# Kernel optimization log

Hardware: AMD Instinct MI355X
Metric: run time of the kernel (lower is better)

## Reference

```python
import jax, jax.numpy as jnp
import numpy as np

B, H, S, D = 2, 16, 2048, 64

def setup_inputs() -> dict:
    key = jax.random.key(0)
    kq, kk, kv, km = jax.random.split(key, 4)
    Q = jax.random.normal(kq, (B, H, S, D), dtype=jnp.float32)
    K = jax.random.normal(kk, (B, H, S, D), dtype=jnp.float32)
    V = jax.random.normal(kv, (B, H, S, D), dtype=jnp.float32)
    # padding-style boolean mask, broadcast over heads; True = masked out
    attn_mask = jax.random.randint(km, (B, 1, S, S), 0, 2).astype(jnp.bool_)
    return {"Q": Q, "K": K, "V": V, "attn_mask": attn_mask}

def reference(Q, K, V, attn_mask):
    d = Q.shape[-1]
    scale = 1.0 / np.sqrt(d).astype(np.float32)
    # [B,H,S,S] scores
    scores = jnp.einsum('bhqd,bhkd->bhqk', Q, K) * scale
    scores = jnp.where(attn_mask, jnp.float32(-1e9), scores)
    attn = jax.nn.softmax(scores, axis=-1)
    context = jnp.einsum('bhqk,bhkd->bhqd', attn, V)
    return context
```

## Files before the change

### kernel.cpp

```cpp
#include <hip/hip_runtime.h>

#define B_ 2
#define H_ 16
#define S_ 2048
#define D_ 64
#define BK 32
#define NKT (S_ / BK)
#define QSCALE 0.18033688011112042f

#define KSD 36
#define VTD 18
#define KS_SZ (BK * KSD)
#define VT_SZ (D_ * VTD)

typedef __attribute__((ext_vector_type(4))) float  float4v;
typedef __attribute__((ext_vector_type(2))) _Float16 half2v;
typedef __attribute__((ext_vector_type(4))) _Float16 half4v;
typedef __attribute__((ext_vector_type(8))) _Float16 half8v;
typedef __attribute__((ext_vector_type(2))) __fp16 fp16x2;
typedef __attribute__((ext_vector_type(2))) unsigned uint2v;

union H2U { half2v h; fp16x2 g; unsigned u; };
union H4U { half4v h4; half2v h2[2]; fp16x2 g2[2]; uint2v u2; };
union H8U { half8v h8; half2v h2[4]; fp16x2 g2[4]; };

__device__ __forceinline__ unsigned pkh(float a, float b) {
    H2U c; c.g = __builtin_amdgcn_cvt_pkrtz(a, b);
    return c.u;
}
__device__ __forceinline__ float fexp2(float x) {
#if __has_builtin(__builtin_amdgcn_exp2f)
    return __builtin_amdgcn_exp2f(x);
#else
    return exp2f(x);
#endif
}

struct Stage { float4 k0, k1, va, vb; };

__device__ __forceinline__ void stage_load(const float* __restrict__ Kg,
                                           const float* __restrict__ Vg,
                                           int kk, int dd, int kp, Stage& s) {
    s.k0 = *(const float4*)(Kg + (size_t)kk * D_ + dd);
    s.k1 = *(const float4*)(Kg + (size_t)(kk + 16) * D_ + dd);
    s.va = *(const float4*)(Vg + (size_t)(2 * kp) * D_ + dd);
    s.vb = *(const float4*)(Vg + (size_t)(2 * kp + 1) * D_ + dd);
}

__device__ __forceinline__ void stage_store(unsigned* KsB, unsigned* VtB,
                                            int kwa, int kwb, const int* vw,
                                            const Stage& s) {
    *(uint2v*)&KsB[kwa] = (uint2v){ pkh(s.k0.x, s.k0.y), pkh(s.k0.z, s.k0.w) };
    *(uint2v*)&KsB[kwb] = (uint2v){ pkh(s.k1.x, s.k1.y), pkh(s.k1.z, s.k1.w) };
    VtB[vw[0]] = pkh(s.va.x, s.vb.x);
    VtB[vw[1]] = pkh(s.va.y, s.vb.y);
    VtB[vw[2]] = pkh(s.va.z, s.vb.z);
    VtB[vw[3]] = pkh(s.va.w, s.vb.w);
}

__global__ __launch_bounds__(256, 4)
void attn_flash_st(const float* __restrict__ Q, const float* __restrict__ K,
                   const float* __restrict__ V, const int* __restrict__ mask,
                   float* __restrict__ out)
{
    __shared__ unsigned KsAll[2 * KS_SZ];
    __shared__ unsigned VtAll[2 * VT_SZ];

    const int tid  = threadIdx.x;
    const int lane = tid & 63;
    const int wave = tid >> 6;
    const int l15  = lane & 15;
    const int quad = lane >> 4;
    const int bh   = blockIdx.y;
    const int b    = bh / H_;
    const int qbase = blockIdx.x * 64 + wave * 16;
    const size_t qkv = (size_t)bh * S_ * D_;

    half8v qf[2];
    {
        const float* qrow = Q + qkv + (size_t)(qbase + l15) * D_ + quad * 8;
        #pragma unroll
        for (int dc = 0; dc < 2; ++dc) {
            float4 f0 = *(const float4*)(qrow + dc * 32);
            float4 f1 = *(const float4*)(qrow + dc * 32 + 4);
            H8U u;
            u.g2[0] = __builtin_amdgcn_cvt_pkrtz(f0.x * QSCALE, f0.y * QSCALE);
            u.g2[1] = __builtin_amdgcn_cvt_pkrtz(f0.z * QSCALE, f0.w * QSCALE);
            u.g2[2] = __builtin_amdgcn_cvt_pkrtz(f1.x * QSCALE, f1.y * QSCALE);
            u.g2[3] = __builtin_amdgcn_cvt_pkrtz(f1.z * QSCALE, f1.w * QSCALE);
            qf[dc] = u.h8;
        }
    }

    const int kk = tid >> 4;
    const int dd = (tid & 15) * 4;
    const int kwa = kk * KSD + (tid & 15) * 2;
    const int kwb = (kk + 16) * KSD + (tid & 15) * 2;
    int vw[4];
    #pragma unroll
    for (int m = 0; m < 4; ++m)
        vw[m] = (dd + m) * VTD + (kk ^ (((dd + m) & 7) << 1));

    int kroff[2][2];
    #pragma unroll
    for (int t = 0; t < 2; ++t)
        #pragma unroll
        for (int dc = 0; dc < 2; ++dc)
            kroff[t][dc] = (t * 16 + l15) * KSD + dc * 16 + quad * 4;
    const int vswz = (l15 & 7) << 1;
    const int p0x[2] = { (quad * 2) ^ vswz, (8 + quad * 2) ^ vswz };
    int vrow[4];
    #pragma unroll
    for (int nb = 0; nb < 4; ++nb) vrow[nb] = (nb * 16 + l15) * VTD;

    const int* mrow = mask + (size_t)b * S_ * S_ + (size_t)(qbase + l15) * S_ + quad * 4;

    float m_run = -INFINITY, l_run = 0.0f;
    float4v o[4];
    #pragma unroll
    for (int nb = 0; nb < 4; ++nb) o[nb] = (float4v){0.f, 0.f, 0.f, 0.f};

    const float* Kg0 = K + qkv;
    const float* Vg0 = V + qkv;

    Stage cur;
    stage_load(Kg0, Vg0, kk, dd, kk, cur);
    stage_store(KsAll, VtAll, kwa, kwb, vw, cur);
    __syncthreads();

    for (int kt = 0; kt < NKT; ++kt) {
        const int buf = kt & 1;
        const unsigned* KsB = KsAll + buf * KS_SZ;
        const unsigned* VtB = VtAll + buf * VT_SZ;

        const int ktn = (kt + 1 < NKT) ? kt + 1 : NKT - 1;
        Stage nxt;
        stage_load(Kg0 + (size_t)ktn * BK * D_, Vg0 + (size_t)ktn * BK * D_, kk, dd, kk, nxt);

        float4v st0 = (float4v){0.f,0.f,0.f,0.f}, st1 = st0;
        {
            half8v kf;
            kf = *(const half8v*)&KsB[kroff[0][0]];
            st0 = __builtin_amdgcn_mfma_f32_16x16x32_f16(kf, qf[0], st0, 0, 0, 0);
            kf = *(const half8v*)&KsB[kroff[0][1]];
            st0 = __builtin_amdgcn_mfma_f32_16x16x32_f16(kf, qf[1], st0, 0, 0, 0);
            kf = *(const half8v*)&KsB[kroff[1][0]];
            st1 = __builtin_amdgcn_mfma_f32_16x16x32_f16(kf, qf[0], st1, 0, 0, 0);
            kf = *(const half8v*)&KsB[kroff[1][1]];
            st1 = __builtin_amdgcn_mfma_f32_16x16x32_f16(kf, qf[1], st1, 0, 0, 0);
        }

        const int4 mk0 = *(const int4*)(mrow);
        const int4 mk1 = *(const int4*)(mrow + 16);
        mrow += BK;
        st0.x = mk0.x ? -1e9f : st0.x;  st0.y = mk0.y ? -1e9f : st0.y;
        st0.z = mk0.z ? -1e9f : st0.z;  st0.w = mk0.w ? -1e9f : st0.w;
        st1.x = mk1.x ? -1e9f : st1.x;  st1.y = mk1.y ? -1e9f : st1.y;
        st1.z = mk1.z ? -1e9f : st1.z;  st1.w = mk1.w ? -1e9f : st1.w;

        float mx = fmaxf(fmaxf(fmaxf(st0.x, st0.y), fmaxf(st0.z, st0.w)),
                         fmaxf(fmaxf(st1.x, st1.y), fmaxf(st1.z, st1.w)));
        mx = fmaxf(mx, __shfl_xor(mx, 16, 64));
        mx = fmaxf(mx, __shfl_xor(mx, 32, 64));
        const float mnew = fmaxf(m_run, mx);
        const float alpha = fexp2(m_run - mnew);
        m_run = mnew;

        st0.x = fexp2(st0.x - mnew); st0.y = fexp2(st0.y - mnew);
        st0.z = fexp2(st0.z - mnew); st0.w = fexp2(st0.w - mnew);
        st1.x = fexp2(st1.x - mnew); st1.y = fexp2(st1.y - mnew);
        st1.z = fexp2(st1.z - mnew); st1.w = fexp2(st1.w - mnew);

        float ls = ((st0.x + st0.y) + (st0.z + st0.w)) +
                   ((st1.x + st1.y) + (st1.z + st1.w));
        ls += __shfl_xor(ls, 16, 64);
        ls += __shfl_xor(ls, 32, 64);
        l_run = l_run * alpha + ls;

        #pragma unroll
        for (int nb = 0; nb < 4; ++nb) o[nb] *= alpha;

        H4U pf0u, pf1u;
        pf0u.g2[0] = __builtin_amdgcn_cvt_pkrtz(st0.x, st0.y);
        pf0u.g2[1] = __builtin_amdgcn_cvt_pkrtz(st0.z, st0.w);
        pf1u.g2[0] = __builtin_amdgcn_cvt_pkrtz(st1.x, st1.y);
        pf1u.g2[1] = __builtin_amdgcn_cvt_pkrtz(st1.z, st1.w);

        #pragma unroll
        for (int nb = 0; nb < 4; ++nb) {
            H4U vf;
            vf.u2 = *(const uint2v*)&VtB[vrow[nb] + p0x[0]];
            o[nb] = __builtin_amdgcn_mfma_f32_16x16x16f16(vf.h4, pf0u.h4, o[nb], 0, 0, 0);
            vf.u2 = *(const uint2v*)&VtB[vrow[nb] + p0x[1]];
            o[nb] = __builtin_amdgcn_mfma_f32_16x16x16f16(vf.h4, pf1u.h4, o[nb], 0, 0, 0);
        }

        stage_store((unsigned*)KsAll + (buf ^ 1) * KS_SZ,
                    (unsigned*)VtAll + (buf ^ 1) * VT_SZ, kwa, kwb, vw, nxt);
        __syncthreads();
    }

    const float inv = 1.0f / l_run;
    float* orow = out + qkv + (size_t)(qbase + l15) * D_ + quad * 4;
    #pragma unroll
    for (int nb = 0; nb < 4; ++nb) {
        float4 ov = { o[nb].x * inv, o[nb].y * inv, o[nb].z * inv, o[nb].w * inv };
        *(float4*)(orow + nb * 16) = ov;
    }
}

extern "C" void kernel_launch(void* const* d_in, const int* in_sizes, int n_in,
                              void* d_out, int out_size, void* d_ws, size_t ws_size,
                              hipStream_t stream) {
    const float* Q    = (const float*)d_in[0];
    const float* K    = (const float*)d_in[1];
    const float* V    = (const float*)d_in[2];
    const int*   mask = (const int*)d_in[3];
    float* out = (float*)d_out;

    dim3 grid(S_ / 64, B_ * H_);
    dim3 block(256);
    attn_flash_st<<<grid, block, 0, stream>>>(Q, K, V, mask, out);
}
```

Before: 233.7 us.

## Deepen K/V global prefetch to two tiles and prefetch mask one tile ahead

Global loads of K/V are issued two tiles ahead into alternating register stages, and mask loads are issued one iteration early so their latency overlaps the MFMA work. The V-transpose LDS swizzle is changed to depend on the column block rather than the low row bits, and the per-block read offsets are precomputed. __syncthreads is replaced by an inline s_waitcnt lgkmcnt(0) plus s_barrier that skips waiting on outstanding global loads. This raises register pressure from the extra staged tile and depends on the new swizzle staying consistent between writes and reads.

```diff
diff --git a/kernel.cpp b/kernel.cpp
--- a/kernel.cpp
+++ b/kernel.cpp
@@ -22,7 +22,7 @@
 
 union H2U { half2v h; fp16x2 g; unsigned u; };
 union H4U { half4v h4; half2v h2[2]; fp16x2 g2[2]; uint2v u2; };
-union H8U { half8v h8; half2v h2[4]; fp16x2 g2[4]; };
+union H8U { half8v h8; fp16x2 g2[4]; };
 
 __device__ __forceinline__ unsigned pkh(float a, float b) {
     H2U c; c.g = __builtin_amdgcn_cvt_pkrtz(a, b);
@@ -36,15 +36,19 @@
 #endif
 }
 
+__device__ __forceinline__ void wg_barrier() {
+    asm volatile("s_waitcnt lgkmcnt(0)\n\ts_barrier" ::: "memory");
+}
+
 struct Stage { float4 k0, k1, va, vb; };
 
 __device__ __forceinline__ void stage_load(const float* __restrict__ Kg,
                                            const float* __restrict__ Vg,
-                                           int kk, int dd, int kp, Stage& s) {
+                                           int kk, int dd, Stage& s) {
     s.k0 = *(const float4*)(Kg + (size_t)kk * D_ + dd);
     s.k1 = *(const float4*)(Kg + (size_t)(kk + 16) * D_ + dd);
-    s.va = *(const float4*)(Vg + (size_t)(2 * kp) * D_ + dd);
-    s.vb = *(const float4*)(Vg + (size_t)(2 * kp + 1) * D_ + dd);
+    s.va = *(const float4*)(Vg + (size_t)(2 * kk) * D_ + dd);
+    s.vb = *(const float4*)(Vg + (size_t)(2 * kk + 1) * D_ + dd);
 }
 
 __device__ __forceinline__ void stage_store(unsigned* KsB, unsigned* VtB,
@@ -68,9 +72,9 @@
 
     const int tid  = threadIdx.x;
     const int lane = tid & 63;
-    const int wave = tid >> 6;
     const int l15  = lane & 15;
     const int quad = lane >> 4;
+    const int wave = tid >> 6;
     const int bh   = blockIdx.y;
     const int b    = bh / H_;
     const int qbase = blockIdx.x * 64 + wave * 16;
@@ -99,7 +103,7 @@
     int vw[4];
     #pragma unroll
     for (int m = 0; m < 4; ++m)
-        vw[m] = (dd + m) * VTD + (kk ^ (((dd + m) & 7) << 1));
+        vw[m] = (dd + m) * VTD + (kk ^ ((((dd + m) >> 4) & 3) << 1));
 
     int kroff[2][2];
     #pragma unroll
@@ -107,13 +111,14 @@
         #pragma unroll
         for (int dc = 0; dc < 2; ++dc)
             kroff[t][dc] = (t * 16 + l15) * KSD + dc * 16 + quad * 4;
-    const int vswz = (l15 & 7) << 1;
-    const int p0x[2] = { (quad * 2) ^ vswz, (8 + quad * 2) ^ vswz };
-    int vrow[4];
-    #pragma unroll
-    for (int nb = 0; nb < 4; ++nb) vrow[nb] = (nb * 16 + l15) * VTD;
-
-    const int* mrow = mask + (size_t)b * S_ * S_ + (size_t)(qbase + l15) * S_ + quad * 4;
+    int vrd[4][2];
+    #pragma unroll
+    for (int nb = 0; nb < 4; ++nb)
+        #pragma unroll
+        for (int t = 0; t < 2; ++t)
+            vrd[nb][t] = (nb * 16 + l15) * VTD + ((t * 8 + quad * 2) ^ ((nb & 3) << 1));
+
+    const int* mrow0 = mask + (size_t)b * S_ * S_ + (size_t)(qbase + l15) * S_ + quad * 4;
 
     float m_run = -INFINITY, l_run = 0.0f;
     float4v o[4];
@@ -123,19 +128,25 @@
     const float* Kg0 = K + qkv;
     const float* Vg0 = V + qkv;
 
-    Stage cur;
-    stage_load(Kg0, Vg0, kk, dd, kk, cur);
-    stage_store(KsAll, VtAll, kwa, kwb, vw, cur);
-    __syncthreads();
+    Stage sl[2];
+    stage_load(Kg0, Vg0, kk, dd, sl[0]);
+    stage_store(KsAll, VtAll, kwa, kwb, vw, sl[0]);
+    stage_load(Kg0 + BK * D_, Vg0 + BK * D_, kk, dd, sl[1]);
+    int4 mk0 = *(const int4*)(mrow0);
+    int4 mk1 = *(const int4*)(mrow0 + 16);
+    wg_barrier();
 
     for (int kt = 0; kt < NKT; ++kt) {
         const int buf = kt & 1;
         const unsigned* KsB = KsAll + buf * KS_SZ;
         const unsigned* VtB = VtAll + buf * VT_SZ;
 
-        const int ktn = (kt + 1 < NKT) ? kt + 1 : NKT - 1;
-        Stage nxt;
-        stage_load(Kg0 + (size_t)ktn * BK * D_, Vg0 + (size_t)ktn * BK * D_, kk, dd, kk, nxt);
+        const int ktn = (kt + 2 < NKT) ? kt + 2 : NKT - 1;
+        stage_load(Kg0 + (size_t)ktn * BK * D_, Vg0 + (size_t)ktn * BK * D_, kk, dd, sl[buf]);
+        const int mtn = (kt + 1 < NKT) ? kt + 1 : NKT - 1;
+        const int* mnext = mrow0 + (size_t)mtn * BK;
+        const int4 nm0 = *(const int4*)(mnext);
+        const int4 nm1 = *(const int4*)(mnext + 16);
 
         float4v st0 = (float4v){0.f,0.f,0.f,0.f}, st1 = st0;
         {
@@ -150,9 +161,6 @@
             st1 = __builtin_amdgcn_mfma_f32_16x16x32_f16(kf, qf[1], st1, 0, 0, 0);
         }
 
-        const int4 mk0 = *(const int4*)(mrow);
-        const int4 mk1 = *(const int4*)(mrow + 16);
-        mrow += BK;
         st0.x = mk0.x ? -1e9f : st0.x;  st0.y = mk0.y ? -1e9f : st0.y;
         st0.z = mk0.z ? -1e9f : st0.z;  st0.w = mk0.w ? -1e9f : st0.w;
         st1.x = mk1.x ? -1e9f : st1.x;  st1.y = mk1.y ? -1e9f : st1.y;
@@ -189,15 +197,16 @@
         #pragma unroll
         for (int nb = 0; nb < 4; ++nb) {
             H4U vf;
-            vf.u2 = *(const uint2v*)&VtB[vrow[nb] + p0x[0]];
+            vf.u2 = *(const uint2v*)&VtB[vrd[nb][0]];
             o[nb] = __builtin_amdgcn_mfma_f32_16x16x16f16(vf.h4, pf0u.h4, o[nb], 0, 0, 0);
-            vf.u2 = *(const uint2v*)&VtB[vrow[nb] + p0x[1]];
+            vf.u2 = *(const uint2v*)&VtB[vrd[nb][1]];
             o[nb] = __builtin_amdgcn_mfma_f32_16x16x16f16(vf.h4, pf1u.h4, o[nb], 0, 0, 0);
         }
 
         stage_store((unsigned*)KsAll + (buf ^ 1) * KS_SZ,
-                    (unsigned*)VtAll + (buf ^ 1) * VT_SZ, kwa, kwb, vw, nxt);
-        __syncthreads();
+                    (unsigned*)VtAll + (buf ^ 1) * VT_SZ, kwa, kwb, vw, sl[buf ^ 1]);
+        wg_barrier();
+        mk0 = nm0; mk1 = nm1;
     }
 
     const float inv = 1.0f / l_run;
```

After: 583.5 us. 150% more time.
